# Kernel optimization log

Measured on AMD Instinct MI355X. Metric: run time of the kernel, lower is better.

The kernel has to match this reference:

```python
import jax, jax.numpy as jnp
import numpy as np

EPS = 1e-16

def setup_inputs() -> dict:
    key = jax.random.key(0)
    u = jax.random.normal(key, (16, 1024, 1024, 1), dtype=jnp.float32)
    return {"u": u}

def reference(u) -> jnp.ndarray:
    # Reflect-pad H and W by 1 (matches tf.pad mode='REFLECT').
    p = jnp.pad(u, ((0, 0), (1, 1), (1, 1), (0, 0)), mode='reflect')
    c = p[:, 1:-1, 1:-1, :]  # center = u
    # The six 3x3 'convs' are shift-subtract stencils (TF conv = correlation):
    dxf = p[:, 2:, 1:-1, :] - c                          # dxforward:  u[i+1,j]-u[i,j]
    dxb = c - p[:, :-2, 1:-1, :]                         # dxback:     u[i,j]-u[i-1,j]
    dyf = p[:, 1:-1, 2:, :] - c                          # dyforward:  u[i,j+1]-u[i,j]
    dyb = c - p[:, 1:-1, :-2, :]                         # dybackward: u[i,j]-u[i,j-1]
    dsbf = p[:, :-2, 2:, :] - p[:, :-2, 1:-1, :]         # dystepbackforward
    dslf = p[:, 2:, :-2, :] - p[:, 1:-1, :-2, :]         # dxstepleftforward
    F = jnp.sqrt(dxf * dxf + dyf * dyf + EPS)
    G = jnp.sqrt(dxb * dxb + dsbf * dsbf + EPS)
    H = jnp.sqrt(dslf * dslf + dyb * dyb + EPS)
    return dxf / F - dxb / G + dyf / F - dyb / H
```

## Files before the change

kernel.cpp:

```cpp
#include <hip/hip_runtime.h>
#include <hip/hip_bf16.h>


#define Wdim 1024
#define Hdim 1024
#define EPSf 1e-16f

__global__ __launch_bounds__(256) void curv_kernel(const float* __restrict__ u,
                                                   float* __restrict__ out) {
    int t = blockIdx.x * blockDim.x + threadIdx.x;
    int q  = t & 255;
    int w0 = q << 2;
    int h  = (t >> 8) & (Hdim - 1);
    int b  = t >> 18;

    const float* base = u + ((size_t)b << 20);
    int hm = (h == 0)        ? 1        : h - 1;
    int hp = (h == Hdim - 1) ? Hdim - 2 : h + 1;

    const float4* rowC = (const float4*)(base + (size_t)h  * Wdim);
    const float4* rowM = (const float4*)(base + (size_t)hm * Wdim);
    const float4* rowP = (const float4*)(base + (size_t)hp * Wdim);

    float4 c4 = rowC[q];
    float4 m4 = rowM[q];
    float4 p4 = rowP[q];

    float cl, pl;
    if (w0 == 0) { cl = c4.y; pl = p4.y; }
    else {
        cl = base[(size_t)h  * Wdim + w0 - 1];
        pl = base[(size_t)hp * Wdim + w0 - 1];
    }
    float cr, mr;
    if (w0 + 4 == Wdim) { cr = c4.z; mr = m4.z; }
    else {
        cr = base[(size_t)h  * Wdim + w0 + 4];
        mr = base[(size_t)hm * Wdim + w0 + 4];
    }

    float c[6] = {cl, c4.x, c4.y, c4.z, c4.w, cr};
    float m[5] = {m4.x, m4.y, m4.z, m4.w, mr};
    float p[5] = {pl, p4.x, p4.y, p4.z, p4.w};

    float4 o;
    float* op = &o.x;
#pragma unroll
    for (int j = 0; j < 4; ++j) {
        float cc   = c[j + 1];
        float cyp  = c[j + 2];
        float cym  = c[j];
        float mm   = m[j];
        float myp  = m[j + 1];
        float pp   = p[j + 1];
        float pym  = p[j];

        float dxf  = pp  - cc;
        float dxb  = cc  - mm;
        float dyf  = cyp - cc;
        float dyb  = cc  - cym;
        float dsbf = myp - mm;
        float dslf = pym - cym;

        float invF = rsqrtf(dxf * dxf + dyf * dyf + EPSf);
        float invG = rsqrtf(dxb * dxb + dsbf * dsbf + EPSf);
        float invH = rsqrtf(dslf * dslf + dyb * dyb + EPSf);

        op[j] = (dxf + dyf) * invF - dxb * invG - dyb * invH;
    }

    ((float4*)out)[t] = o;
}

extern "C" void kernel_launch(void* const* d_in, const int* in_sizes, int n_in,
                              void* d_out, int out_size, void* d_ws, size_t ws_size,
                              hipStream_t stream) {
    const float* u = (const float*)d_in[0];
    float* out = (float*)d_out;
    int total = in_sizes[0];
    int n4 = total >> 2;
    int blocks = n4 / 256;
    curv_kernel<<<blocks, 256, 0, stream>>>(u, out);
}
```

Baseline: 130.5 us.

## Compute four rows per thread and swizzle block order across XCDs

Each thread now loads six rows once (four output rows plus a halo row on each side) and writes four rows. This replaces the three row loads per output row in the old code, so vertical neighbour data is reused in registers. Block indices are also remapped so that consecutive blocks land on the same XCD and touch adjacent memory, which should help L2 locality. In exchange the grid is hardcoded to 4096 blocks and each thread uses more registers.

```diff
diff --git a/kernel.cpp b/kernel.cpp
--- a/kernel.cpp
+++ b/kernel.cpp
@@ -8,68 +8,74 @@
 
 __global__ __launch_bounds__(256) void curv_kernel(const float* __restrict__ u,
                                                    float* __restrict__ out) {
-    int t = blockIdx.x * blockDim.x + threadIdx.x;
-    int q  = t & 255;
+    int blk = ((blockIdx.x & 7) << 9) | (blockIdx.x >> 3);
+    int q  = threadIdx.x;
     int w0 = q << 2;
-    int h  = (t >> 8) & (Hdim - 1);
-    int b  = t >> 18;
+    int rowBlk = blk & 255;
+    int b      = blk >> 8;
+    int r0     = rowBlk << 2;
 
     const float* base = u + ((size_t)b << 20);
-    int hm = (h == 0)        ? 1        : h - 1;
-    int hp = (h == Hdim - 1) ? Hdim - 2 : h + 1;
 
-    const float4* rowC = (const float4*)(base + (size_t)h  * Wdim);
-    const float4* rowM = (const float4*)(base + (size_t)hm * Wdim);
-    const float4* rowP = (const float4*)(base + (size_t)hp * Wdim);
+    int rIdx[6];
+    rIdx[0] = (r0 == 0) ? 1 : r0 - 1;
+    rIdx[1] = r0;
+    rIdx[2] = r0 + 1;
+    rIdx[3] = r0 + 2;
+    rIdx[4] = r0 + 3;
+    rIdx[5] = (r0 + 4 == Hdim) ? Hdim - 2 : r0 + 4;
 
-    float4 c4 = rowC[q];
-    float4 m4 = rowM[q];
-    float4 p4 = rowP[q];
+    float4 R[6];
+#pragma unroll
+    for (int k = 0; k < 6; ++k)
+        R[k] = ((const float4*)(base + (size_t)rIdx[k] * Wdim))[q];
 
-    float cl, pl;
-    if (w0 == 0) { cl = c4.y; pl = p4.y; }
-    else {
-        cl = base[(size_t)h  * Wdim + w0 - 1];
-        pl = base[(size_t)hp * Wdim + w0 - 1];
-    }
-    float cr, mr;
-    if (w0 + 4 == Wdim) { cr = c4.z; mr = m4.z; }
-    else {
-        cr = base[(size_t)h  * Wdim + w0 + 4];
-        mr = base[(size_t)hm * Wdim + w0 + 4];
-    }
+    bool le = (w0 == 0), re = (w0 + 4 == Wdim);
+    float Lv[6], Rv[6];
+#pragma unroll
+    for (int k = 1; k < 6; ++k)
+        Lv[k] = le ? R[k].y : base[(size_t)rIdx[k] * Wdim + w0 - 1];
+#pragma unroll
+    for (int k = 0; k < 5; ++k)
+        Rv[k] = re ? R[k].z : base[(size_t)rIdx[k] * Wdim + w0 + 4];
 
-    float c[6] = {cl, c4.x, c4.y, c4.z, c4.w, cr};
-    float m[5] = {m4.x, m4.y, m4.z, m4.w, mr};
-    float p[5] = {pl, p4.x, p4.y, p4.z, p4.w};
-
-    float4 o;
-    float* op = &o.x;
+    size_t obase = ((size_t)b << 20) + (size_t)r0 * Wdim;
 #pragma unroll
     for (int j = 0; j < 4; ++j) {
-        float cc   = c[j + 1];
-        float cyp  = c[j + 2];
-        float cym  = c[j];
-        float mm   = m[j];
-        float myp  = m[j + 1];
-        float pp   = p[j + 1];
-        float pym  = p[j];
+        const float4& C = R[1 + j];
+        const float4& M = R[j];
+        const float4& P = R[2 + j];
+        float c[6] = {Lv[1 + j], C.x, C.y, C.z, C.w, Rv[1 + j]};
+        float m[5] = {M.x, M.y, M.z, M.w, Rv[j]};
+        float p[5] = {Lv[2 + j], P.x, P.y, P.z, P.w};
 
-        float dxf  = pp  - cc;
-        float dxb  = cc  - mm;
-        float dyf  = cyp - cc;
-        float dyb  = cc  - cym;
-        float dsbf = myp - mm;
-        float dslf = pym - cym;
+        float4 o;
+        float* op = &o.x;
+#pragma unroll
+        for (int i = 0; i < 4; ++i) {
+            float cc   = c[i + 1];
+            float cyp  = c[i + 2];
+            float cym  = c[i];
+            float mm   = m[i];
+            float myp  = m[i + 1];
+            float pp   = p[i + 1];
+            float pym  = p[i];
 
-        float invF = rsqrtf(dxf * dxf + dyf * dyf + EPSf);
-        float invG = rsqrtf(dxb * dxb + dsbf * dsbf + EPSf);
-        float invH = rsqrtf(dslf * dslf + dyb * dyb + EPSf);
+            float dxf  = pp  - cc;
+            float dxb  = cc  - mm;
+            float dyf  = cyp - cc;
+            float dyb  = cc  - cym;
+            float dsbf = myp - mm;
+            float dslf = pym - cym;
 
-        op[j] = (dxf + dyf) * invF - dxb * invG - dyb * invH;
+            float invF = rsqrtf(dxf * dxf + dyf * dyf + EPSf);
+            float invG = rsqrtf(dxb * dxb + dsbf * dsbf + EPSf);
+            float invH = rsqrtf(dslf * dslf + dyb * dyb + EPSf);
+
+            op[i] = (dxf + dyf) * invF - dxb * invG - dyb * invH;
+        }
+        ((float4*)(out + obase + (size_t)j * Wdim))[q] = o;
     }
-
-    ((float4*)out)[t] = o;
 }
 
 extern "C" void kernel_launch(void* const* d_in, const int* in_sizes, int n_in,
@@ -77,8 +83,5 @@
                               hipStream_t stream) {
     const float* u = (const float*)d_in[0];
     float* out = (float*)d_out;
-    int total = in_sizes[0];
-    int n4 = total >> 2;
-    int blocks = n4 / 256;
-    curv_kernel<<<blocks, 256, 0, stream>>>(u, out);
+    curv_kernel<<<4096, 256, 0, stream>>>(u, out);
 }
```

Result: faster. 121.6 us (-6.8%).
